# Kernel optimization log

Hardware: AMD Instinct MI355X
Metric: run time of the kernel (lower is better)

The kernel has to match this reference:

```python
import jax, jax.numpy as jnp
import numpy as np

B, S, DIN, DIM = 4, 4096, 256, 256
GAMMA = 0.9865


def setup_inputs() -> dict:
    key = jax.random.key(0)
    ks = jax.random.split(key, 9)
    inp = {
        'xq': jax.random.normal(ks[0], (B, S, DIN), dtype=jnp.float32),
        'xk': jax.random.normal(ks[1], (B, S, DIN), dtype=jnp.float32),
        'xv': jax.random.normal(ks[2], (B, S, DIN), dtype=jnp.float32),
        'Wq': jax.random.normal(ks[3], (DIN, DIM), dtype=jnp.float32) * 0.05,
        'bq': jnp.zeros((DIM,), dtype=jnp.float32),
        'Wk': jax.random.normal(ks[4], (DIN, DIM), dtype=jnp.float32) * 0.05,
        'bk': jnp.zeros((DIM,), dtype=jnp.float32),
        'Wv': jax.random.normal(ks[5], (DIN, DIM), dtype=jnp.float32) * 0.05,
        'bv': jnp.zeros((DIM,), dtype=jnp.float32),
    }
    return inp


def _decay_matrix(s, gamma):
    # D[i, j] = gamma^(i-j) if i >= j else 0
    idx = jnp.arange(s)
    diff = idx[:, None] - idx[None, :]
    D = jnp.where(diff >= 0,
                  jnp.power(jnp.float32(gamma), diff.astype(jnp.float32)),
                  jnp.float32(0.0))
    return D


def reference(xq, xk, xv, Wq, bq, Wk, bk, Wv, bv):
    Q = xq @ Wq + bq  # [B,S,D]
    K = xk @ Wk + bk  # [B,S,D]
    V = xv @ Wv + bv  # [B,S,D]
    d = Q.shape[-1]
    # scores[b,i,j] = Q[b,i] . K[b,j] / sqrt(d)
    x = jnp.einsum('bid,bjd->bij', Q, K) / jnp.sqrt(jnp.float32(d))
    D = _decay_matrix(S, GAMMA)
    # Faithful to TF broadcasting: divides along the LAST axis (per-column by
    # sqrt of that index's row-sum): D[i,j] /= sqrt(sum_k D[j,k])
    D = D / jnp.sqrt(jnp.sum(D, axis=-1))
    x = x * D  # broadcast [B,S,S] * [S,S]
    # _norm_3 per batch element with TF broadcasting: x[b,i,j] /= max(|sum_k x[b,j,k]|, 1)
    denom = jnp.maximum(jnp.abs(jnp.sum(x, axis=-1)), 1.0)  # [B,S]
    x = x / denom[:, None, :]
    return x @ V  # [B,S,D]
```

## Files before the change

kernel.cpp:

```cpp
#include <hip/hip_runtime.h>
#include <math.h>

#define BB 4
#define SS 4096
#define DD 256
#define LL 256
#define NCH 16
#define GAMMA 0.9865f
#define LOG2G (-0.019609034f)
#define INV1MG 74.07407407f
#define SLAB 1032
#define SLABB 520

typedef __attribute__((ext_vector_type(8))) short short8;
typedef __attribute__((ext_vector_type(4))) float f32x4;
typedef unsigned short u16;
typedef unsigned int u32;

__device__ __forceinline__ u16 f2bf(float f) {
  union { float f; unsigned u; } v; v.f = f;
  unsigned r = v.u + 0x7FFFu + ((v.u >> 16) & 1u);
  return (u16)(r >> 16);
}
__device__ __forceinline__ float bf2f(u16 h) {
  union { unsigned u; float f; } v; v.u = ((unsigned)h) << 16; return v.f;
}

__device__ __forceinline__ void gll16(const u16* g, u16* l) {
  __builtin_amdgcn_global_load_lds(
      (const __attribute__((address_space(1))) u32*)g,
      (__attribute__((address_space(3))) u32*)l, 16, 0, 0);
}
__device__ __forceinline__ void stage8kp(const u16* g, u16* l, int lane) {
#pragma unroll
  for (int i = 0; i < 8; ++i)
    gll16(g + i * 512 + lane * 8, l + (i >> 1) * SLAB + (i & 1) * 512);
}

__device__ __forceinline__ void mfma_step_regB(
    const u16* Ah, const u16* Al, const short8 bh[4], const short8 bl[4],
    int wm0, int fm, int fq, f32x4 acc[4][4])
{
  const int ka = fq * SLAB;
  short8 ah[4], al[4];
#pragma unroll
  for (int i = 0; i < 4; ++i) {
    ah[i] = *(const short8*)&Ah[ka + (wm0 + i * 16 + fm) * 8];
    al[i] = *(const short8*)&Al[ka + (wm0 + i * 16 + fm) * 8];
  }
#pragma unroll
  for (int j = 0; j < 4; ++j)
#pragma unroll
    for (int i = 0; i < 4; ++i) {
      acc[i][j] = __builtin_amdgcn_mfma_f32_16x16x32_bf16(al[i], bh[j], acc[i][j], 0, 0, 0);
      acc[i][j] = __builtin_amdgcn_mfma_f32_16x16x32_bf16(ah[i], bl[j], acc[i][j], 0, 0, 0);
      acc[i][j] = __builtin_amdgcn_mfma_f32_16x16x32_bf16(ah[i], bh[j], acc[i][j], 0, 0, 0);
    }
}

__device__ __forceinline__ void mfma_step_regB_ab(
    const u16* Ah, const u16* Al, const short8 bh[2], const short8 bl[2],
    int wm0, int fm, int fq, f32x4 acc[4][2])
{
  const int ka = fq * SLAB;
  short8 ah[4], al[4];
#pragma unroll
  for (int i = 0; i < 4; ++i) {
    ah[i] = *(const short8*)&Ah[ka + (wm0 + i * 16 + fm) * 8];
    al[i] = *(const short8*)&Al[ka + (wm0 + i * 16 + fm) * 8];
  }
#pragma unroll
  for (int j = 0; j < 2; ++j)
#pragma unroll
    for (int i = 0; i < 4; ++i) {
      acc[i][j] = __builtin_amdgcn_mfma_f32_16x16x32_bf16(al[i], bh[j], acc[i][j], 0, 0, 0);
      acc[i][j] = __builtin_amdgcn_mfma_f32_16x16x32_bf16(ah[i], bl[j], acc[i][j], 0, 0, 0);
      acc[i][j] = __builtin_amdgcn_mfma_f32_16x16x32_bf16(ah[i], bh[j], acc[i][j], 0, 0, 0);
    }
}

__device__ __forceinline__ void loadBW(short8 bh[4], short8 bl[4],
    const u16* WhP, const u16* WlP, int ks, int wn0, int fm, int fq)
{
  const int base = ks * 4096 + fq * 1024;
#pragma unroll
  for (int j = 0; j < 4; ++j) {
    int o = base + (wn0 + j * 16 + fm) * 8;
    bh[j] = *(const short8*)&WhP[o];
    bl[j] = *(const short8*)&WlP[o];
  }
}
__device__ __forceinline__ void loadB2(short8 bh[2], short8 bl[2],
    const u16* BhP, const u16* BlP, int ks, int wn0, int fm, int fq)
{
  const int base = ks * 4096 + fq * 1024;
#pragma unroll
  for (int j = 0; j < 2; ++j) {
    int o = base + (wn0 + j * 16 + fm) * 8;
    bh[j] = *(const short8*)&BhP[o];
    bl[j] = *(const short8*)&BlP[o];
  }
}

__device__ __forceinline__ void mfma_step_ab(
    const u16* Ah, const u16* Al, const u16* Bh, const u16* Bl,
    int wm0, int wn0, int fm, int fq, f32x4 acc[4][2])
{
  const int ka = fq * SLAB, kb = fq * SLABB;
  short8 ah[4], al[4];
#pragma unroll
  for (int i = 0; i < 4; ++i) {
    ah[i] = *(const short8*)&Ah[ka + (wm0 + i * 16 + fm) * 8];
    al[i] = *(const short8*)&Al[ka + (wm0 + i * 16 + fm) * 8];
  }
#pragma unroll
  for (int j = 0; j < 2; ++j) {
    short8 bh = *(const short8*)&Bh[kb + (wn0 + j * 16 + fm) * 8];
    short8 bl = *(const short8*)&Bl[kb + (wn0 + j * 16 + fm) * 8];
#pragma unroll
    for (int i = 0; i < 4; ++i) {
      acc[i][j] = __builtin_amdgcn_mfma_f32_16x16x32_bf16(al[i], bh, acc[i][j], 0, 0, 0);
      acc[i][j] = __builtin_amdgcn_mfma_f32_16x16x32_bf16(ah[i], bl, acc[i][j], 0, 0, 0);
      acc[i][j] = __builtin_amdgcn_mfma_f32_16x16x32_bf16(ah[i], bh, acc[i][j], 0, 0, 0);
    }
  }
}

__device__ __forceinline__ void bounce_write(
    float* fb, const f32x4 acc[4][4], int wm0, int wn0, int fm, int fq, int p)
{
  if (wn0 == p * 64) {
#pragma unroll
    for (int i = 0; i < 4; ++i)
#pragma unroll
      for (int j = 0; j < 4; ++j)
#pragma unroll
        for (int r = 0; r < 4; ++r)
          fb[(wm0 + i * 16 + fq * 4 + r) * 65 + j * 16 + fm] = acc[i][j][r];
  }
}

__global__ __launch_bounds__(256) void init_pack_kernel(
    const float* __restrict__ Wq, const float* __restrict__ Wk, const float* __restrict__ Wv,
    u16* __restrict__ Wth, u16* __restrict__ Wtl,
    float* __restrict__ rsP, float* __restrict__ lVec)
{
  const int which = blockIdx.x;
  const int it = blockIdx.y;
  const int t = threadIdx.x;
  if (which == 0) {
    *(float4*)&rsP[(size_t)(it * 256 + t) * 4] = (float4){0.f, 0.f, 0.f, 0.f};
  } else if (which == 1) {
    *(float4*)&lVec[(size_t)(it * 256 + t) * 4] = (float4){0.f, 0.f, 0.f, 0.f};
  }
  const float* W = which == 0 ? Wq : (which == 1 ? Wk : Wv);
  for (int pn = 0; pn < 2; ++pn) {
    int pos = it * 256 + t;
    int k8 = pos >> 7, r = pos & 127;
    u16 hs[8], ls[8];
#pragma unroll
    for (int u = 0; u < 8; ++u) {
      float x = W[(size_t)(k8 * 8 + u) * DD + pn * 128 + r];
      u16 h = f2bf(x); hs[u] = h; ls[u] = f2bf(x - bf2f(h));
    }
    size_t o = ((size_t)((which * 2 + pn) * 32 + k8)) * 1024 + (size_t)r * 8;
    *(short8*)&Wth[o] = *(short8*)hs;
    *(short8*)&Wtl[o] = *(short8*)ls;
  }
}

__device__ __forceinline__ void loadX(float xs[2][8], const float* XP, int ks,
                                      int arow, int ak8) {
#pragma unroll
  for (int t = 0; t < 2; ++t) {
    const float* src = XP + (size_t)(t * 64 + arow) * DD + ks * 32 + ak8 * 8;
    *(float4*)&xs[t][0] = *(const float4*)src;
    *(float4*)&xs[t][4] = *(const float4*)(src + 4);
  }
}
__device__ __forceinline__ void writeAsplit(u16* Ab, const float xs[2][8],
                                            int arow, int ak8) {
#pragma unroll
  for (int t = 0; t < 2; ++t) {
    int row = t * 64 + arow;
    u16 hs[8], ls[8];
#pragma unroll
    for (int u = 0; u < 8; ++u) {
      u16 h = f2bf(xs[t][u]); hs[u] = h; ls[u] = f2bf(xs[t][u] - bf2f(h));
    }
    *(short8*)&Ab[ak8 * SLAB + row * 8] = *(short8*)hs;
    *(short8*)&Ab[4 * SLAB + ak8 * SLAB + row * 8] = *(short8*)ls;
  }
}

__global__ __launch_bounds__(256, 3) void proj_kernel(
    const float* __restrict__ xq, const float* __restrict__ xk, const float* __restrict__ xv,
    const u16* __restrict__ Wth, const u16* __restrict__ Wtl,
    const float* __restrict__ bq, const float* __restrict__ bk_, const float* __restrict__ bv,
    u16* __restrict__ Qh, u16* __restrict__ Ql,
    u16* __restrict__ Kh, u16* __restrict__ Kl,
    u16* __restrict__ KTh, u16* __restrict__ KTl, float* __restrict__ VT32,
    float* __restrict__ lVec)
{
  const int which = blockIdx.z;
  const float* bias = which == 0 ? bq : (which == 1 ? bk_ : bv);
  const int m0 = blockIdx.x * 128;
  const int pn = blockIdx.y;
  __shared__ u16 SM[16 * SLAB + 128];
  __shared__ float rsc[128];
  __shared__ float wlut[128];
  __shared__ float kacc[64];
  float* fb = (float*)SM;
  const int tid = threadIdx.x, lane = tid & 63, wave = tid >> 6;
  const int wm0 = (wave >> 1) * 64, wn0 = (wave & 1) * 64;
  const int fm = lane & 15, fq = lane >> 4;
  if (which == 1) {
    if (tid < 128) {
      int sb = (m0 & (SS - 1)) + tid;
      rsc[tid] = rsqrtf((1.0f - exp2f((float)(sb + 1) * LOG2G)) * INV1MG);
      wlut[tid] = exp2f((float)(255 - ((m0 & (LL - 1)) + tid)) * LOG2G);
    }
    if (tid < 64) kacc[tid] = 0.f;
  }
  const float* XP = (which == 0 ? xq : (which == 1 ? xk : xv)) + (size_t)m0 * DD;
  const u16* WhP = Wth + (size_t)((which * 2 + pn) * 32) * 1024;
  const u16* WlP = Wtl + (size_t)((which * 2 + pn) * 32) * 1024;
  const int arow = tid >> 2, ak8 = tid & 3;
  f32x4 acc[4][4];
#pragma unroll
  for (int i = 0; i < 4; ++i)
#pragma unroll
    for (int j = 0; j < 4; ++j) acc[i][j] = (f32x4){0.f, 0.f, 0.f, 0.f};
  float xs[2][8];
  short8 bh[4], bl[4];
  loadBW(bh, bl, WhP, WlP, 0, wn0, fm, fq);
  loadX(xs, XP, 0, arow, ak8);
  writeAsplit(SM, xs, arow, ak8);
  int cur = 0;
  for (int ks = 0; ks < 8; ++ks) {
    __syncthreads();
    u16* Ac = SM + cur * 8 * SLAB;
    u16* An = SM + (cur ^ 1) * 8 * SLAB;
    if (ks < 7) loadX(xs, XP, ks + 1, arow, ak8);
    mfma_step_regB(Ac, Ac + 4 * SLAB, bh, bl, wm0, fm, fq, acc);
    if (ks < 7) {
      loadBW(bh, bl, WhP, WlP, ks + 1, wn0, fm, fq);
      writeAsplit(An, xs, arow, ak8);
    }
    cur ^= 1;
  }
  const int b = m0 >> 12, sbb = m0 & (SS - 1);
  for (int p = 0; p < 2; ++p) {
    __syncthreads();
    bounce_write(fb, acc, wm0, wn0, fm, fq, p);
    __syncthreads();
    if (which == 0) {
#pragma unroll
      for (int it = 0; it < 4; ++it) {
        int unit = it * 256 + tid;
        int k8l = unit >> 7, row = unit & 127;
        int gcol0 = pn * 128 + p * 64 + k8l * 8;
        u16 hs[8], ls[8];
#pragma unroll
        for (int u = 0; u < 8; ++u) {
          float v = (fb[row * 65 + k8l * 8 + u] + bias[gcol0 + u]) * (1.f / 16.f);
          u16 h = f2bf(v); hs[u] = h; ls[u] = f2bf(v - bf2f(h));
        }
        size_t o = (size_t)(m0 >> 7) * 32768 + (size_t)(pn * 16 + p * 8 + k8l) * 1024 + row * 8;
        *(short8*)&Qh[o] = *(short8*)hs;
        *(short8*)&Ql[o] = *(short8*)ls;
      }
    } else if (which == 1) {
#pragma unroll
      for (int it = 0; it < 4; ++it) {
        int unit = it * 256 + tid;
        int k8l = unit >> 7, row = unit & 127;
        int gcol0 = pn * 128 + p * 64 + k8l * 8;
        u16 hs[8], ls[8];
#pragma unroll
        for (int u = 0; u < 8; ++u) {
          float v = (fb[row * 65 + k8l * 8 + u] + bias[gcol0 + u]) * rsc[row];
          u16 h = f2bf(v); hs[u] = h; ls[u] = f2bf(v - bf2f(h));
        }
        size_t o = (size_t)(m0 >> 7) * 32768 + (size_t)(pn * 16 + p * 8 + k8l) * 1024 + row * 8;
        *(short8*)&Kh[o] = *(short8*)hs;
        *(short8*)&Kl[o] = *(short8*)ls;
      }
      float kpart = 0.f;
#pragma unroll
      for (int it = 0; it < 4; ++it) {
        int unit = it * 256 + tid;
        int dl = unit & 63, s8l = unit >> 6;
        int gcolg = pn * 128 + p * 64 + dl;
        float bs = bias[gcolg];
        u16 hs[8], ls[8];
#pragma unroll
        for (int u = 0; u < 8; ++u) {
          int row = s8l * 8 + u;
          float v = (fb[row * 65 + dl] + bs) * rsc[row];
          kpart = fmaf(v, wlut[row], kpart);
          u16 h = f2bf(v); hs[u] = h; ls[u] = f2bf(v - bf2f(h));
        }
        int sb0 = sbb + s8l * 8;
        size_t o = ((size_t)(b * 2 + (gcolg >> 7)) * 512 + (sb0 >> 3)) * 1024 + (size_t)(gcolg & 127) * 8;
        *(short8*)&KTh[o] = *(short8*)hs;
        *(short8*)&KTl[o] = *(short8*)ls;
      }
      atomicAdd(&kacc[tid & 63], kpart);
      __syncthreads();
      if (tid < 64) {
        int c = sbb >> 8;
        atomicAdd(&lVec[(size_t)(b * NCH + c) * DD + pn * 128 + p * 64 + tid], kacc[tid]);
        kacc[tid] = 0.f;
      }
    } else {
#pragma unroll
      for (int it = 0; it < 4; ++it) {
        int unit = it * 256 + tid;
        int dl = unit & 63, s8l = unit >> 6;
        int gcolg = pn * 128 + p * 64 + dl;
        float bs = bias[gcolg];
        float vv[8];
#pragma unroll
        for (int u = 0; u < 8; ++u) vv[u] = fb[(s8l * 8 + u) * 65 + dl] + bs;
        float* dst = &VT32[(size_t)b * DD * SS + (size_t)gcolg * SS + sbb + s8l * 8];
        *(float4*)dst = (float4){vv[0], vv[1], vv[2], vv[3]};
        *(float4*)(dst + 4) = (float4){vv[4], vv[5], vv[6], vv[7]};
      }
    }
  }
}

__global__ __launch_bounds__(256, 4) void scores_kernel(
    const u16* __restrict__ Qh, const u16* __restrict__ Ql,
    const u16* __restrict__ Kh, const u16* __restrict__ Kl,
    const float* __restrict__ lVec, u16* __restrict__ Sgh, u16* __restrict__ Sgl,
    float* __restrict__ rsP)
{
  const int chunk = blockIdx.x, b = chunk >> 4, c = chunk & 15;
  const int y = blockIdx.y;
  const int m0 = (y < 2) ? 0 : 128;
  const int jn0 = (y < 2) ? y * 64 : (y - 2) * 64;
  __shared__ u16 SA[2 * 8 * SLAB];
  __shared__ float cv[256], lut[256], rowAcc[128], qd2[2][128];
  float* fb = (float*)SA;
  const int tid = threadIdx.x, lane = tid & 63, wave = tid >> 6;
  const int wm0 = (wave >> 1) * 64, wn0 = (wave & 1) * 32;
  const int fm = lane & 15, fq = lane >> 4;
  if (jn0 == 0) {
    const float gL = exp2f((float)LL * LOG2G);
    float s = 0.f;
    for (int cp = 0; cp < c; ++cp)
      s = fmaf(gL, s, lVec[(size_t)(b * NCH + cp) * DD + tid]);
    cv[tid] = s;
  }
  lut[tid] = exp2f((float)tid * LOG2G);
  if (tid < 128) rowAcc[tid] = 0.f;
  const int growA = b * SS + c * LL + m0;
  const int growB = b * SS + c * LL + jn0;
  const u16* QhP = Qh + (size_t)(growA >> 7) * 32768;
  const u16* QlP = Ql + (size_t)(growA >> 7) * 32768;
  const u16* KhP = Kh + (size_t)(growB >> 7) * 32768 + (size_t)(growB & 127) * 8;
  const u16* KlP = Kl + (size_t)(growB >> 7) * 32768 + (size_t)(growB & 127) * 8;
  f32x4 acc[4][2];
#pragma unroll
  for (int i = 0; i < 4; ++i)
#pragma unroll
    for (int j = 0; j < 2; ++j) acc[i][j] = (f32x4){0.f, 0.f, 0.f, 0.f};
  float qdreg = 0.f;
  const int qrow = tid & 127, qk8b = tid >> 7;
  short8 bh[2], bl[2];
  if (wave == 0) stage8kp(QhP, SA, lane);
  if (wave == 1) stage8kp(QlP, SA + 4 * SLAB, lane);
  loadB2(bh, bl, KhP, KlP, 0, wn0, fm, fq);
  int cur = 0;
  for (int ks = 0; ks < 8; ++ks) {
    __syncthreads();
    u16* Ac = cur ? SA + 8 * SLAB : SA;
    u16* An = cur ? SA : SA + 8 * SLAB;
    if (ks < 7) {
      if (wave == 0) stage8kp(QhP + (ks + 1) * 4096, An, lane);
      if (wave == 1) stage8kp(QlP + (ks + 1) * 4096, An + 4 * SLAB, lane);
    }
    mfma_step_regB_ab(Ac, Ac + 4 * SLAB, bh, bl, wm0, fm, fq, acc);
    if (ks < 7) loadB2(bh, bl, KhP, KlP, ks + 1, wn0, fm, fq);
    if (jn0 == 0) {
#pragma unroll
      for (int h2 = 0; h2 < 2; ++h2) {
        int k8l = qk8b + 2 * h2;
        const u16* ahp = &Ac[k8l * SLAB + qrow * 8];
        const u16* alp = &Ac[4 * SLAB + k8l * SLAB + qrow * 8];
#pragma unroll
        for (int u = 0; u < 8; ++u)
          qdreg = fmaf(bf2f(ahp[u]) + bf2f(alp[u]), cv[ks * 32 + k8l * 8 + u], qdreg);
      }
    }
    cur ^= 1;
  }
  qd2[qk8b][qrow] = qdreg;
  const int ps = chunk * 2 + (m0 >> 7);
  for (int rh = 0; rh < 2; ++rh) {
    __syncthreads();
    if (wm0 == rh * 64) {
#pragma unroll
      for (int i = 0; i < 4; ++i)
#pragma unroll
        for (int j = 0; j < 2; ++j)
#pragma unroll
          for (int r = 0; r < 4; ++r)
            fb[(i * 16 + fq * 4 + r) * 65 + wn0 + j * 16 + fm] = acc[i][j][r];
    }
    __syncthreads();
#pragma unroll
    for (int it = 0; it < 2; ++it) {
      int unit = it * 256 + tid;
      int k8l = unit >> 6, rowl = unit & 63;
      int il = m0 + rh * 64 + rowl;
      int jlb = jn0 + k8l * 8;
      float part = 0.f;
      u16 hs[8], ls[8];
#pragma unroll
      for (int u = 0; u < 8; ++u) {
        int jl = jlb + u;
        float v = (jl <= il) ? fb[rowl * 65 + k8l * 8 + u] * lut[il - jl] : 0.f;
        part += v;
        u16 h = f2bf(v); hs[u] = h; ls[u] = f2bf(v - bf2f(h));
      }
      atomicAdd(&rowAcc[rh * 64 + rowl], part);
      size_t o = (size_t)(ps * 32 + (jn0 >> 3) + k8l) * 1024 + (size_t)(rh * 64 + rowl) * 8;
      *(short8*)&Sgh[o] = *(short8*)hs;
      *(short8*)&Sgl[o] = *(short8*)ls;
    }
  }
  __syncthreads();
  if (tid < 128) {
    float rs = rowAcc[tid];
    if (jn0 == 0)
      rs += exp2f((float)(m0 + tid + 1) * LOG2G) * (qd2[0][tid] + qd2[1][tid]);
    atomicAdd(&rsP[(size_t)b * SS + c * LL + m0 + tid], rs);
  }
}

__global__ __launch_bounds__(256, 4) void lmat_kernel(
    const float* __restrict__ VT32, const float* __restrict__ rsP,
    const u16* __restrict__ KTh, const u16* __restrict__ KTl,
    float* __restrict__ lMatT)
{
  const int chunk = blockIdx.x, b = chunk >> 4, c = chunk & 15;
  const int ty = blockIdx.y;
  const int m0 = (ty >> 2) * 128, n0 = (ty & 3) * 64;
  __shared__ u16 SA[2 * 8 * SLAB];
  __shared__ float swl[256];
  const int tid = threadIdx.x, lane = tid & 63, wave = tid >> 6;
  const int wm0 = (wave >> 1) * 64, wn0 = (wave & 1) * 32;
  const int fm = lane & 15, fq = lane >> 4;
  swl[tid] = exp2f((float)(255 - tid) * LOG2G) /
             fmaxf(fabsf(rsP[(size_t)b * SS + c * LL + tid]), 1.0f);
  const float* AP = VT32 + (size_t)b * DD * SS + (size_t)m0 * SS + c * LL;
  const u16* BhP = KTh + ((size_t)(b * 2 + (n0 >> 7)) * 512 + c * 32) * 1024 + (size_t)(n0 & 127) * 8;
  const u16* BlP = KTl + ((size_t)(b * 2 + (n0 >> 7)) * 512 + c * 32) * 1024 + (size_t)(n0 & 127) * 8;
  const int arow = tid >> 1;
  f32x4 acc[4][2];
#pragma unroll
  for (int i = 0; i < 4; ++i)
#pragma unroll
    for (int j = 0; j < 2; ++j) acc[i][j] = (f32x4){0.f, 0.f, 0.f, 0.f};
  float as[2][8];
  short8 bh[2], bl[2];
  loadB2(bh, bl, BhP, BlP, 0, wn0, fm, fq);
#pragma unroll
  for (int t = 0; t < 2; ++t) {
    int ak8 = (tid & 1) * 2 + t;
    const float* src = AP + (size_t)arow * SS + ak8 * 8;
    *(float4*)&as[t][0] = *(const float4*)src;
    *(float4*)&as[t][4] = *(const float4*)(src + 4);
  }
  __syncthreads();
#pragma unroll
  for (int t = 0; t < 2; ++t) {
    int ak8 = (tid & 1) * 2 + t;
    u16 hs[8], ls[8];
#pragma unroll
    for (int u = 0; u < 8; ++u) {
      float v = as[t][u] * swl[ak8 * 8 + u];
      u16 h = f2bf(v); hs[u] = h; ls[u] = f2bf(v - bf2f(h));
    }
    *(short8*)&SA[ak8 * SLAB + arow * 8] = *(short8*)hs;
    *(short8*)&SA[4 * SLAB + ak8 * SLAB + arow * 8] = *(short8*)ls;
  }
  int cur = 0;
  for (int ks = 0; ks < 8; ++ks) {
    __syncthreads();
    u16* Ac = cur ? SA + 8 * SLAB : SA;
    u16* An = cur ? SA : SA + 8 * SLAB;
    if (ks < 7) {
#pragma unroll
      for (int t = 0; t < 2; ++t) {
        int ak8 = (tid & 1) * 2 + t;
        const float* src = AP + (size_t)arow * SS + (ks + 1) * 32 + ak8 * 8;
        *(float4*)&as[t][0] = *(const float4*)src;
        *(float4*)&as[t][4] = *(const float4*)(src + 4);
      }
    }
    mfma_step_regB_ab(Ac, Ac + 4 * SLAB, bh, bl, wm0, fm, fq, acc);
    if (ks < 7) {
      loadB2(bh, bl, BhP, BlP, ks + 1, wn0, fm, fq);
#pragma unroll
      for (int t = 0; t < 2; ++t) {
        int ak8 = (tid & 1) * 2 + t;
        u16 hs[8], ls[8];
#pragma unroll
        for (int u = 0; u < 8; ++u) {
          float v = as[t][u] * swl[(ks + 1) * 32 + ak8 * 8 + u];
          u16 h = f2bf(v); hs[u] = h; ls[u] = f2bf(v - bf2f(h));
        }
        *(short8*)&An[ak8 * SLAB + arow * 8] = *(short8*)hs;
        *(short8*)&An[4 * SLAB + ak8 * SLAB + arow * 8] = *(short8*)ls;
      }
    }
    cur ^= 1;
  }
#pragma unroll
  for (int i = 0; i < 4; ++i)
#pragma unroll
    for (int j = 0; j < 2; ++j)
#pragma unroll
      for (int r = 0; r < 4; ++r) {
        int e = m0 + wm0 + i * 16 + fq * 4 + r;
        int d = n0 + wn0 + j * 16 + fm;
        lMatT[(size_t)chunk * 65536 + (size_t)e * 256 + d] = acc[i][j][r];
      }
}

__global__ __launch_bounds__(256) void combine_mat_kernel(
    const float* __restrict__ lMatT, u16* __restrict__ cMh, u16* __restrict__ cMl)
{
  const int t = blockIdx.x * 256 + threadIdx.x;
  const int b = t >> 13, rem = t & 8191;
  const int k8 = rem >> 8, e = rem & 255;
  const float gL = powf(GAMMA, (float)LL);
  float s[8] = {0.f, 0.f, 0.f, 0.f, 0.f, 0.f, 0.f, 0.f};
  for (int ch = 0; ch < 16; ++ch) {
    size_t ro = (size_t)(b * 16 + ch) * 65536 + (size_t)e * 256 + k8 * 8;
    float4 a0 = *(const float4*)&lMatT[ro];
    float4 a1 = *(const float4*)&lMatT[ro + 4];
    float vals[8] = {a0.x, a0.y, a0.z, a0.w, a1.x, a1.y, a1.z, a1.w};
    u16 hh[8], ll[8];
#pragma unroll
    for (int u = 0; u < 8; ++u) {
      u16 h = f2bf(s[u]); hh[u] = h; ll[u] = f2bf(s[u] - bf2f(h));
    }
    size_t wo = ((size_t)(((b * 16 + ch) * 2 + (e >> 7)) * 32 + k8)) * 1024 + (size_t)(e & 127) * 8;
    *(short8*)&cMh[wo] = *(short8*)hh;
    *(short8*)&cMl[wo] = *(short8*)ll;
#pragma unroll
    for (int u = 0; u < 8; ++u) s[u] = gL * s[u] + vals[u];
  }
}

__global__ __launch_bounds__(256, 3) void out_kernel(
    const u16* __restrict__ Qh, const u16* __restrict__ Ql,
    const u16* __restrict__ cMh, const u16* __restrict__ cMl,
    const u16* __restrict__ Sgh, const u16* __restrict__ Sgl,
    const float* __restrict__ VT32, const float* __restrict__ rsP,
    float* __restrict__ out)
{
  const int chunk = blockIdx.x, b = chunk >> 4, c = chunk & 15;
  const int ty = blockIdx.y;
  const int m0 = (ty >> 2) * 128, n0 = (ty & 3) * 64;
  __shared__ u16 SA[2 * 8 * SLAB];
  __shared__ u16 SB[2 * 8 * SLABB];
  __shared__ float olut[128];
  __shared__ float sdn[256];
  const int tid = threadIdx.x, lane = tid & 63, wave = tid >> 6;
  const int wm0 = (wave >> 1) * 64, wn0 = (wave & 1) * 32;
  const int fm = lane & 15, fq = lane >> 4;
  if (tid < 128) olut[tid] = exp2f((float)(m0 + tid + 1) * LOG2G);
  sdn[tid] = 1.0f / fmaxf(fabsf(rsP[(size_t)b * SS + c * LL + tid]), 1.0f);
  f32x4 acc[4][2];
#pragma unroll
  for (int i = 0; i < 4; ++i)
#pragma unroll
    for (int j = 0; j < 2; ++j) acc[i][j] = (f32x4){0.f, 0.f, 0.f, 0.f};
  int cur = 0;
  {
    const u16* AhP = Qh + (size_t)(b * 32 + c * 2 + (m0 >> 7)) * 32768;
    const u16* AlP = Ql + (size_t)(b * 32 + c * 2 + (m0 >> 7)) * 32768;
    const u16* BhP = cMh + (size_t)(chunk * 2 + (n0 >> 7)) * 32768 + (size_t)(n0 & 127) * 8;
    const u16* BlP = cMl + (size_t)(chunk * 2 + (n0 >> 7)) * 32768 + (size_t)(n0 & 127) * 8;
    short8 bh[2], bl[2];
    if (wave == 0) stage8kp(AhP, SA, lane);
    if (wave == 1) stage8kp(AlP, SA + 4 * SLAB, lane);
    loadB2(bh, bl, BhP, BlP, 0, wn0, fm, fq);
    for (int ks = 0; ks < 8; ++ks) {
      __syncthreads();
      u16* Ac = cur ? SA + 8 * SLAB : SA;
      u16* An = cur ? SA : SA + 8 * SLAB;
      if (ks < 7) {
        if (wave == 0) stage8kp(AhP + (ks + 1) * 4096, An, lane);
        if (wave == 1) stage8kp(AlP + (ks + 1) * 4096, An + 4 * SLAB, lane);
      }
      mfma_step_regB_ab(Ac, Ac + 4 * SLAB, bh, bl, wm0, fm, fq, acc);
      if (ks < 7) loadB2(bh, bl, BhP, BlP, ks + 1, wn0, fm, fq);
      cur ^= 1;
    }
  }
  {
    const u16* AhP = Sgh + (size_t)(chunk * 2 + (m0 >> 7)) * 32768;
    const u16* AlP = Sgl + (size_t)(chunk * 2 + (m0 >> 7)) * 32768;
    const float* BP = VT32 + (size_t)b * DD * SS + (size_t)n0 * SS + c * LL;
    const int ber = tid >> 2, bk8 = tid & 3;
    const int nks = (m0 >> 5) + 4;
    float bs[8];
    {
      u16* Ac = cur ? SA + 8 * SLAB : SA;
      u16* Bc = cur ? SB + 8 * SLABB : SB;
      if (wave == 0) stage8kp(AhP, Ac, lane);
      if (wave == 1) stage8kp(AlP, Ac + 4 * SLAB, lane);
      const float* src = BP + (size_t)ber * SS + bk8 * 8;
      *(float4*)&bs[0] = *(const float4*)src;
      *(float4*)&bs[4] = *(const float4*)(src + 4);
#pragma unroll
      for (int i = 0; i < 4; ++i)
#pragma unroll
        for (int r = 0; r < 4; ++r) {
          int rl = wm0 + i * 16 + fq * 4 + r;
          float sc = olut[rl];
#pragma unroll
          for (int j = 0; j < 2; ++j) acc[i][j][r] *= sc;
        }
      u16 hs[8], ls[8];
#pragma unroll
      for (int u = 0; u < 8; ++u) {
        float v = bs[u] * sdn[bk8 * 8 + u];
        u16 h = f2bf(v); hs[u] = h; ls[u] = f2bf(v - bf2f(h));
      }
      *(short8*)&Bc[bk8 * SLABB + ber * 8] = *(short8*)hs;
      *(short8*)&Bc[4 * SLABB + bk8 * SLABB + ber * 8] = *(short8*)ls;
    }
    for (int ks = 0; ks < nks; ++ks) {
      __syncthreads();
      u16* Ac = cur ? SA + 8 * SLAB : SA;
      u16* Bc = cur ? SB + 8 * SLABB : SB;
      u16* An = cur ? SA : SA + 8 * SLAB;
      u16* Bn = cur ? SB : SB + 8 * SLABB;
      if (ks + 1 < nks) {
        if (wave == 0) stage8kp(AhP + (ks + 1) * 4096, An, lane);
        if (wave == 1) stage8kp(AlP + (ks + 1) * 4096, An + 4 * SLAB, lane);
        const float* src = BP + (size_t)ber * SS + (ks + 1) * 32 + bk8 * 8;
        *(float4*)&bs[0] = *(const float4*)src;
        *(float4*)&bs[4] = *(const float4*)(src + 4);
      }
      mfma_step_ab(Ac, Ac + 4 * SLAB, Bc, Bc + 4 * SLABB, wm0, wn0, fm, fq, acc);
      if (ks + 1 < nks) {
        u16 hs[8], ls[8];
#pragma unroll
        for (int u = 0; u < 8; ++u) {
          float v = bs[u] * sdn[(ks + 1) * 32 + bk8 * 8 + u];
          u16 h = f2bf(v); hs[u] = h; ls[u] = f2bf(v - bf2f(h));
        }
        *(short8*)&Bn[bk8 * SLABB + ber * 8] = *(short8*)hs;
        *(short8*)&Bn[4 * SLABB + bk8 * SLABB + ber * 8] = *(short8*)ls;
      }
      cur ^= 1;
    }
  }
#pragma unroll
  for (int i = 0; i < 4; ++i)
#pragma unroll
    for (int j = 0; j < 2; ++j)
#pragma unroll
      for (int r = 0; r < 4; ++r) {
        int il = m0 + wm0 + i * 16 + fq * 4 + r;
        int e = n0 + wn0 + j * 16 + fm;
        out[(size_t)(b * SS + c * LL + il) * DD + e] = acc[i][j][r];
      }
}

extern "C" void kernel_launch(void* const* d_in, const int* in_sizes, int n_in,
                              void* d_out, int out_size, void* d_ws, size_t ws_size,
                              hipStream_t stream) {
  const float* xq = (const float*)d_in[0];
  const float* xk = (const float*)d_in[1];
  const float* xv = (const float*)d_in[2];
  const float* Wq = (const float*)d_in[3];
  const float* bq = (const float*)d_in[4];
  const float* Wk = (const float*)d_in[5];
  const float* bk = (const float*)d_in[6];
  const float* Wv = (const float*)d_in[7];
  const float* bv = (const float*)d_in[8];
  float* out = (float*)d_out;

  char* p = (char*)d_ws;
  const size_t H16 = (size_t)BB * SS * DD * 2;
  u16* Qh   = (u16*)(p + 0 * H16);  u16* Ql   = (u16*)(p + 1 * H16);
  u16* Kh   = (u16*)(p + 2 * H16);  u16* Kl   = (u16*)(p + 3 * H16);
  u16* KTh  = (u16*)(p + 4 * H16);  u16* KTl  = (u16*)(p + 5 * H16);
  u16* Sgh  = (u16*)(p + 10 * H16); u16* Sgl  = (u16*)(p + 11 * H16);
  u16* cMh  = (u16*)(p + 12 * H16); u16* cMl  = (u16*)(p + 13 * H16);
  float* lMatT = (float*)(p + 14 * H16);
  float* VT32  = (float*)(p + 16 * H16);
  u16* Wth = (u16*)(p + 18 * H16);
  u16* Wtl = (u16*)(p + 18 * H16 + 3 * DD * DD * 2);
  float* rsP  = (float*)(p + 18 * H16 + 6 * DD * DD * 2);
  float* lVec = rsP + (size_t)BB * SS;

  init_pack_kernel<<<dim3(3, 16), 256, 0, stream>>>(Wq, Wk, Wv, Wth, Wtl, rsP, lVec);
  proj_kernel<<<dim3(BB * SS / 128, 2, 3), 256, 0, stream>>>(
      xq, xk, xv, Wth, Wtl, bq, bk, bv, Qh, Ql, Kh, Kl, KTh, KTl, VT32, lVec);
  scores_kernel<<<dim3(BB * NCH, 6), 256, 0, stream>>>(
      Qh, Ql, Kh, Kl, lVec, Sgh, Sgl, rsP);
  lmat_kernel<<<dim3(BB * NCH, 8), 256, 0, stream>>>(VT32, rsP, KTh, KTl, lMatT);
  combine_mat_kernel<<<128, 256, 0, stream>>>(lMatT, cMh, cMl);
  out_kernel<<<dim3(BB * NCH, 8), 256, 0, stream>>>(
      Qh, Ql, cMh, cMl, Sgh, Sgl, VT32, rsP, out);
}
```

Baseline: 198.2 us.

## Load A operands straight from global into registers instead of LDS staging

Removes the global_load_lds double-buffered staging of the Q/Sg A-tiles in scores_kernel and out_kernel. Each wave now loads its A fragments directly from global memory into registers every k-step, and the first GEMM phase no longer needs barriers. This shrinks LDS use and eliminates per-step syncs. Launch bounds are raised to 4 blocks per CU for proj and out kernels to take advantage, at the cost of more global/L2 traffic, since fragments shared across waves are now loaded redundantly, and exposed load latency with no prefetching.

```diff
diff --git a/kernel.cpp b/kernel.cpp
--- a/kernel.cpp
+++ b/kernel.cpp
@@ -26,17 +26,6 @@
   union { unsigned u; float f; } v; v.u = ((unsigned)h) << 16; return v.f;
 }
 
-__device__ __forceinline__ void gll16(const u16* g, u16* l) {
-  __builtin_amdgcn_global_load_lds(
-      (const __attribute__((address_space(1))) u32*)g,
-      (__attribute__((address_space(3))) u32*)l, 16, 0, 0);
-}
-__device__ __forceinline__ void stage8kp(const u16* g, u16* l, int lane) {
-#pragma unroll
-  for (int i = 0; i < 8; ++i)
-    gll16(g + i * 512 + lane * 8, l + (i >> 1) * SLAB + (i & 1) * 512);
-}
-
 __device__ __forceinline__ void mfma_step_regB(
     const u16* Ah, const u16* Al, const short8 bh[4], const short8 bl[4],
     int wm0, int fm, int fq, f32x4 acc[4][4])
@@ -58,17 +47,10 @@
     }
 }
 
-__device__ __forceinline__ void mfma_step_regB_ab(
-    const u16* Ah, const u16* Al, const short8 bh[2], const short8 bl[2],
-    int wm0, int fm, int fq, f32x4 acc[4][2])
-{
-  const int ka = fq * SLAB;
-  short8 ah[4], al[4];
-#pragma unroll
-  for (int i = 0; i < 4; ++i) {
-    ah[i] = *(const short8*)&Ah[ka + (wm0 + i * 16 + fm) * 8];
-    al[i] = *(const short8*)&Al[ka + (wm0 + i * 16 + fm) * 8];
-  }
+__device__ __forceinline__ void mfma_regs_ab(
+    const short8 ah[4], const short8 al[4],
+    const short8 bh[2], const short8 bl[2], f32x4 acc[4][2])
+{
 #pragma unroll
   for (int j = 0; j < 2; ++j)
 #pragma unroll
@@ -79,6 +61,17 @@
     }
 }
 
+__device__ __forceinline__ void loadA4(short8 ah[4], short8 al[4],
+    const u16* AhP, const u16* AlP, int ks, int wm0, int fm, int fq)
+{
+  const int base = ks * 4096 + fq * 1024;
+#pragma unroll
+  for (int i = 0; i < 4; ++i) {
+    int o = base + (wm0 + i * 16 + fm) * 8;
+    ah[i] = *(const short8*)&AhP[o];
+    al[i] = *(const short8*)&AlP[o];
+  }
+}
 __device__ __forceinline__ void loadBW(short8 bh[4], short8 bl[4],
     const u16* WhP, const u16* WlP, int ks, int wn0, int fm, int fq)
 {
@@ -102,17 +95,11 @@
   }
 }
 
-__device__ __forceinline__ void mfma_step_ab(
-    const u16* Ah, const u16* Al, const u16* Bh, const u16* Bl,
-    int wm0, int wn0, int fm, int fq, f32x4 acc[4][2])
-{
-  const int ka = fq * SLAB, kb = fq * SLABB;
-  short8 ah[4], al[4];
-#pragma unroll
-  for (int i = 0; i < 4; ++i) {
-    ah[i] = *(const short8*)&Ah[ka + (wm0 + i * 16 + fm) * 8];
-    al[i] = *(const short8*)&Al[ka + (wm0 + i * 16 + fm) * 8];
-  }
+__device__ __forceinline__ void mfma_regA_ldsB(
+    const short8 ah[4], const short8 al[4], const u16* Bh, const u16* Bl,
+    int wn0, int fm, int fq, f32x4 acc[4][2])
+{
+  const int kb = fq * SLABB;
 #pragma unroll
   for (int j = 0; j < 2; ++j) {
     short8 bh = *(const short8*)&Bh[kb + (wn0 + j * 16 + fm) * 8];
@@ -124,6 +111,20 @@
       acc[i][j] = __builtin_amdgcn_mfma_f32_16x16x32_bf16(ah[i], bh, acc[i][j], 0, 0, 0);
     }
   }
+}
+
+__device__ __forceinline__ void mfma_ldsA_regB(
+    const u16* Ah, const u16* Al, const short8 bh[2], const short8 bl[2],
+    int wm0, int fm, int fq, f32x4 acc[4][2])
+{
+  const int ka = fq * SLAB;
+  short8 ah[4], al[4];
+#pragma unroll
+  for (int i = 0; i < 4; ++i) {
+    ah[i] = *(const short8*)&Ah[ka + (wm0 + i * 16 + fm) * 8];
+    al[i] = *(const short8*)&Al[ka + (wm0 + i * 16 + fm) * 8];
+  }
+  mfma_regs_ab(ah, al, bh, bl, acc);
 }
 
 __device__ __forceinline__ void bounce_write(
@@ -193,7 +194,7 @@
   }
 }
 
-__global__ __launch_bounds__(256, 3) void proj_kernel(
+__global__ __launch_bounds__(256, 4) void proj_kernel(
     const float* __restrict__ xq, const float* __restrict__ xk, const float* __restrict__ xv,
     const u16* __restrict__ Wth, const u16* __restrict__ Wtl,
     const float* __restrict__ bq, const float* __restrict__ bk_, const float* __restrict__ bv,
@@ -341,9 +342,8 @@
   const int y = blockIdx.y;
   const int m0 = (y < 2) ? 0 : 128;
   const int jn0 = (y < 2) ? y * 64 : (y - 2) * 64;
-  __shared__ u16 SA[2 * 8 * SLAB];
+  __shared__ float fb[64 * 65];
   __shared__ float cv[256], lut[256], rowAcc[128], qd2[2][128];
-  float* fb = (float*)SA;
   const int tid = threadIdx.x, lane = tid & 63, wave = tid >> 6;
   const int wm0 = (wave >> 1) * 64, wn0 = (wave & 1) * 32;
   const int fm = lane & 15, fq = lane >> 4;
@@ -369,33 +369,24 @@
     for (int j = 0; j < 2; ++j) acc[i][j] = (f32x4){0.f, 0.f, 0.f, 0.f};
   float qdreg = 0.f;
   const int qrow = tid & 127, qk8b = tid >> 7;
-  short8 bh[2], bl[2];
-  if (wave == 0) stage8kp(QhP, SA, lane);
-  if (wave == 1) stage8kp(QlP, SA + 4 * SLAB, lane);
-  loadB2(bh, bl, KhP, KlP, 0, wn0, fm, fq);
-  int cur = 0;
+  __syncthreads();
   for (int ks = 0; ks < 8; ++ks) {
-    __syncthreads();
-    u16* Ac = cur ? SA + 8 * SLAB : SA;
-    u16* An = cur ? SA : SA + 8 * SLAB;
-    if (ks < 7) {
-      if (wave == 0) stage8kp(QhP + (ks + 1) * 4096, An, lane);
-      if (wave == 1) stage8kp(QlP + (ks + 1) * 4096, An + 4 * SLAB, lane);
-    }
-    mfma_step_regB_ab(Ac, Ac + 4 * SLAB, bh, bl, wm0, fm, fq, acc);
-    if (ks < 7) loadB2(bh, bl, KhP, KlP, ks + 1, wn0, fm, fq);
+    short8 ah[4], al[4], bh[2], bl[2];
+    loadA4(ah, al, QhP, QlP, ks, wm0, fm, fq);
+    loadB2(bh, bl, KhP, KlP, ks, wn0, fm, fq);
+    mfma_regs_ab(ah, al, bh, bl, acc);
     if (jn0 == 0) {
 #pragma unroll
       for (int h2 = 0; h2 < 2; ++h2) {
         int k8l = qk8b + 2 * h2;
-        const u16* ahp = &Ac[k8l * SLAB + qrow * 8];
-        const u16* alp = &Ac[4 * SLAB + k8l * SLAB + qrow * 8];
+        short8 hv = *(const short8*)&QhP[ks * 4096 + k8l * 1024 + qrow * 8];
+        short8 lv = *(const short8*)&QlP[ks * 4096 + k8l * 1024 + qrow * 8];
 #pragma unroll
         for (int u = 0; u < 8; ++u)
-          qdreg = fmaf(bf2f(ahp[u]) + bf2f(alp[u]), cv[ks * 32 + k8l * 8 + u], qdreg);
-      }
-    }
-    cur ^= 1;
+          qdreg = fmaf(bf2f((u16)hv[u]) + bf2f((u16)lv[u]),
+                       cv[ks * 32 + k8l * 8 + u], qdreg);
+      }
+    }
   }
   qd2[qk8b][qrow] = qdreg;
   const int ps = chunk * 2 + (m0 >> 7);
@@ -502,7 +493,7 @@
         *(float4*)&as[t][4] = *(const float4*)(src + 4);
       }
     }
-    mfma_step_regB_ab(Ac, Ac + 4 * SLAB, bh, bl, wm0, fm, fq, acc);
+    mfma_ldsA_regB(Ac, Ac + 4 * SLAB, bh, bl, wm0, fm, fq, acc);
     if (ks < 7) {
       loadB2(bh, bl, BhP, BlP, ks + 1, wn0, fm, fq);
 #pragma unroll
@@ -558,7 +549,7 @@
   }
 }
 
-__global__ __launch_bounds__(256, 3) void out_kernel(
+__global__ __launch_bounds__(256, 4) void out_kernel(
     const u16* __restrict__ Qh, const u16* __restrict__ Ql,
     const u16* __restrict__ cMh, const u16* __restrict__ cMl,
     const u16* __restrict__ Sgh, const u16* __restrict__ Sgl,
@@ -568,7 +559,6 @@
   const int chunk = blockIdx.x, b = chunk >> 4, c = chunk & 15;
   const int ty = blockIdx.y;
   const int m0 = (ty >> 2) * 128, n0 = (ty & 3) * 64;
-  __shared__ u16 SA[2 * 8 * SLAB];
   __shared__ u16 SB[2 * 8 * SLABB];
   __shared__ float olut[128];
   __shared__ float sdn[256];
@@ -582,29 +572,28 @@
   for (int i = 0; i < 4; ++i)
 #pragma unroll
     for (int j = 0; j < 2; ++j) acc[i][j] = (f32x4){0.f, 0.f, 0.f, 0.f};
-  int cur = 0;
+  __syncthreads();
   {
     const u16* AhP = Qh + (size_t)(b * 32 + c * 2 + (m0 >> 7)) * 32768;
     const u16* AlP = Ql + (size_t)(b * 32 + c * 2 + (m0 >> 7)) * 32768;
     const u16* BhP = cMh + (size_t)(chunk * 2 + (n0 >> 7)) * 32768 + (size_t)(n0 & 127) * 8;
     const u16* BlP = cMl + (size_t)(chunk * 2 + (n0 >> 7)) * 32768 + (size_t)(n0 & 127) * 8;
-    short8 bh[2], bl[2];
-    if (wave == 0) stage8kp(AhP, SA, lane);
-    if (wave == 1) stage8kp(AlP, SA + 4 * SLAB, lane);
-    loadB2(bh, bl, BhP, BlP, 0, wn0, fm, fq);
     for (int ks = 0; ks < 8; ++ks) {
-      __syncthreads();
-      u16* Ac = cur ? SA + 8 * SLAB : SA;
-      u16* An = cur ? SA : SA + 8 * SLAB;
-      if (ks < 7) {
-        if (wave == 0) stage8kp(AhP + (ks + 1) * 4096, An, lane);
-        if (wave == 1) stage8kp(AlP + (ks + 1) * 4096, An + 4 * SLAB, lane);
-      }
-      mfma_step_regB_ab(Ac, Ac + 4 * SLAB, bh, bl, wm0, fm, fq, acc);
-      if (ks < 7) loadB2(bh, bl, BhP, BlP, ks + 1, wn0, fm, fq);
-      cur ^= 1;
-    }
-  }
+      short8 ah[4], al[4], bh[2], bl[2];
+      loadA4(ah, al, AhP, AlP, ks, wm0, fm, fq);
+      loadB2(bh, bl, BhP, BlP, ks, wn0, fm, fq);
+      mfma_regs_ab(ah, al, bh, bl, acc);
+    }
+  }
+#pragma unroll
+  for (int i = 0; i < 4; ++i)
+#pragma unroll
+    for (int r = 0; r < 4; ++r) {
+      int rl = wm0 + i * 16 + fq * 4 + r;
+      float sc = olut[rl];
+#pragma unroll
+      for (int j = 0; j < 2; ++j) acc[i][j][r] *= sc;
+    }
   {
     const u16* AhP = Sgh + (size_t)(chunk * 2 + (m0 >> 7)) * 32768;
     const u16* AlP = Sgl + (size_t)(chunk * 2 + (m0 >> 7)) * 32768;
@@ -613,45 +602,31 @@
     const int nks = (m0 >> 5) + 4;
     float bs[8];
     {
-      u16* Ac = cur ? SA + 8 * SLAB : SA;
-      u16* Bc = cur ? SB + 8 * SLABB : SB;
-      if (wave == 0) stage8kp(AhP, Ac, lane);
-      if (wave == 1) stage8kp(AlP, Ac + 4 * SLAB, lane);
       const float* src = BP + (size_t)ber * SS + bk8 * 8;
       *(float4*)&bs[0] = *(const float4*)src;
       *(float4*)&bs[4] = *(const float4*)(src + 4);
-#pragma unroll
-      for (int i = 0; i < 4; ++i)
-#pragma unroll
-        for (int r = 0; r < 4; ++r) {
-          int rl = wm0 + i * 16 + fq * 4 + r;
-          float sc = olut[rl];
-#pragma unroll
-          for (int j = 0; j < 2; ++j) acc[i][j][r] *= sc;
-        }
       u16 hs[8], ls[8];
 #pragma unroll
       for (int u = 0; u < 8; ++u) {
         float v = bs[u] * sdn[bk8 * 8 + u];
         u16 h = f2bf(v); hs[u] = h; ls[u] = f2bf(v - bf2f(h));
       }
-      *(short8*)&Bc[bk8 * SLABB + ber * 8] = *(short8*)hs;
-      *(short8*)&Bc[4 * SLABB + bk8 * SLABB + ber * 8] = *(short8*)ls;
-    }
+      *(short8*)&SB[bk8 * SLABB + ber * 8] = *(short8*)hs;
+      *(short8*)&SB[4 * SLABB + bk8 * SLABB + ber * 8] = *(short8*)ls;
+    }
+    int cur = 0;
     for (int ks = 0; ks < nks; ++ks) {
       __syncthreads();
-      u16* Ac = cur ? SA + 8 * SLAB : SA;
       u16* Bc = cur ? SB + 8 * SLABB : SB;
-      u16* An = cur ? SA : SA + 8 * SLAB;
       u16* Bn = cur ? SB : SB + 8 * SLABB;
       if (ks + 1 < nks) {
-        if (wave == 0) stage8kp(AhP + (ks + 1) * 4096, An, lane);
-        if (wave == 1) stage8kp(AlP + (ks + 1) * 4096, An + 4 * SLAB, lane);
         const float* src = BP + (size_t)ber * SS + (ks + 1) * 32 + bk8 * 8;
         *(float4*)&bs[0] = *(const float4*)src;
         *(float4*)&bs[4] = *(const float4*)(src + 4);
       }
-      mfma_step_ab(Ac, Ac + 4 * SLAB, Bc, Bc + 4 * SLABB, wm0, wn0, fm, fq, acc);
+      short8 ah[4], al[4];
+      loadA4(ah, al, AhP, AlP, ks, wm0, fm, fq);
+      mfma_regA_ldsB(ah, al, Bc, Bc + 4 * SLABB, wn0, fm, fq, acc);
       if (ks + 1 < nks) {
         u16 hs[8], ls[8];
 #pragma unroll
```

New measurement: 227.1 us. 14.6% more time.
